# Optimization experiments

Measured on AMD Instinct MI355X. Metric: run time of the kernel, lower is better.

The kernel has to match this reference:

```python
import jax, jax.numpy as jnp
import numpy as np

B = 16384
N_TABLES = 26
N_ROWS = 100000
D = 64


def _mlp(x, params, last_sigmoid=False):
    n = len(params)
    for i, (w, b) in enumerate(params):
        x = x @ w.T + b
        if last_sigmoid and i == n - 1:
            x = jax.nn.sigmoid(x)
        else:
            x = jax.nn.relu(x)
    return x


def setup_inputs() -> dict:
    key = jax.random.key(0)
    ks = jax.random.split(key, 16)

    def glorot(k, m, n):
        return jax.random.normal(k, (m, n), jnp.float32) * np.sqrt(2.0 / (m + n))

    def bias(k, m):
        return jax.random.normal(k, (m,), jnp.float32) * np.sqrt(1.0 / m)

    return {
        "dense_x": jax.random.normal(ks[0], (B, 13), jnp.float32),
        "lS_i": jax.random.randint(ks[1], (N_TABLES, B), 0, N_ROWS, jnp.int64 if jax.config.jax_enable_x64 else jnp.int32),
        "emb_W": jax.random.normal(ks[2], (N_TABLES, N_ROWS, D), jnp.float32) * np.sqrt(1.0 / N_ROWS),
        "bot_w0": glorot(ks[3], 512, 13), "bot_b0": bias(ks[4], 512),
        "bot_w1": glorot(ks[5], 256, 512), "bot_b1": bias(ks[6], 256),
        "bot_w2": glorot(ks[7], 64, 256), "bot_b2": bias(ks[8], 64),
        "top_w0": glorot(ks[9], 512, 415), "top_b0": bias(ks[10], 512),
        "top_w1": glorot(ks[11], 256, 512), "top_b1": bias(ks[12], 256),
        "top_w2": glorot(ks[13], 1, 256), "top_b2": bias(ks[14], 1),
    }


def reference(dense_x, lS_i, emb_W, bot_w0, bot_b0, bot_w1, bot_b1, bot_w2, bot_b2,
              top_w0, top_b0, top_w1, top_b1, top_w2, top_b2):
    # bottom MLP: [B,13] -> [B,64]
    x = _mlp(dense_x, [(bot_w0, bot_b0), (bot_w1, bot_b1), (bot_w2, bot_b2)])

    # embedding lookups: one index per sample per table (EmbeddingBag sum over bag of 1)
    # emb_W: [T, N, D], lS_i: [T, B] -> ly: [T, B, D]
    ly = jnp.take_along_axis(emb_W, lS_i[:, :, None], axis=1)  # [T, B, D]

    # interaction: T = concat(x, ly) -> [B, 27, D]; Z = T T^T; lower-tri (i>j) flatten
    T = jnp.concatenate([x[None], ly], axis=0).transpose(1, 0, 2)  # [B, 27, D]
    Z = jnp.einsum("bnd,bmd->bnm", T, T)  # [B, 27, 27]
    li, lj = jnp.tril_indices(N_TABLES + 1, k=-1)  # same order as torch list comp
    Zflat = Z[:, li, lj]  # [B, 351]
    R = jnp.concatenate([x, Zflat], axis=1)  # [B, 415]

    # top MLP with sigmoid output
    p = _mlp(R, [(top_w0, top_b0), (top_w1, top_b1), (top_w2, top_b2)], last_sigmoid=True)
    return p
```

## Files before the change

kernel.cpp:

```cpp
#include <hip/hip_runtime.h>
#include <hip/hip_bf16.h>
#include <math.h>


#define BATCH 16384
#define NTAB 26
#define NF 27
#define NROWS 100000
#define EDIM 64
#define PAIRS 351
#define RLD 416

template<int BM, int BN, int BK, int TM, int TN, bool VEC, bool RELU>
__global__ __launch_bounds__(256) void gemm_bias_act(
    const float* __restrict__ A, int lda,
    const float* __restrict__ W, int ldw,
    const float* __restrict__ bias,
    float* __restrict__ C, int ldc,
    int M, int N, int K)
{
    __shared__ float As[BK][BM + 4];
    __shared__ float Ws[BK][BN + 4];

    const int tid  = threadIdx.x;
    const int mblk = blockIdx.x * BM;
    const int nblk = blockIdx.y * BN;

    const int tcol = tid % (BN / TN);
    const int trow = tid / (BN / TN);
    const int m0 = trow * TM;
    const int n0 = tcol * TN;

    float acc[TM][TN];
#pragma unroll
    for (int i = 0; i < TM; ++i)
#pragma unroll
        for (int j = 0; j < TN; ++j) acc[i][j] = 0.f;

    const int ktiles = (K + BK - 1) / BK;
    for (int kt = 0; kt < ktiles; ++kt) {
        const int k0 = kt * BK;
        if (VEC) {
#pragma unroll
            for (int i = 0; i < (BM * BK) / (4 * 256); ++i) {
                int idx = tid + i * 256;
                int am = idx / (BK / 4);
                int a4 = idx % (BK / 4);
                float4 v = *(const float4*)&A[(size_t)(mblk + am) * lda + k0 + a4 * 4];
                As[a4 * 4 + 0][am] = v.x;
                As[a4 * 4 + 1][am] = v.y;
                As[a4 * 4 + 2][am] = v.z;
                As[a4 * 4 + 3][am] = v.w;
            }
#pragma unroll
            for (int i = 0; i < (BN * BK) / (4 * 256); ++i) {
                int idx = tid + i * 256;
                int wn = idx / (BK / 4);
                int w4 = idx % (BK / 4);
                float4 v = *(const float4*)&W[(size_t)(nblk + wn) * ldw + k0 + w4 * 4];
                Ws[w4 * 4 + 0][wn] = v.x;
                Ws[w4 * 4 + 1][wn] = v.y;
                Ws[w4 * 4 + 2][wn] = v.z;
                Ws[w4 * 4 + 3][wn] = v.w;
            }
        } else {
#pragma unroll
            for (int i = 0; i < (BM * BK) / 256; ++i) {
                int idx = tid + i * 256;
                int am = idx / BK;
                int ak = idx % BK;
                int gk = k0 + ak;
                float v = 0.f;
                if (gk < K) v = A[(size_t)(mblk + am) * lda + gk];
                As[ak][am] = v;
            }
#pragma unroll
            for (int i = 0; i < (BN * BK) / 256; ++i) {
                int idx = tid + i * 256;
                int wn = idx / BK;
                int wk = idx % BK;
                int gk = k0 + wk;
                float v = 0.f;
                if (gk < K) v = W[(size_t)(nblk + wn) * ldw + gk];
                Ws[wk][wn] = v;
            }
        }
        __syncthreads();

#pragma unroll
        for (int k = 0; k < BK; ++k) {
            float a[TM], b[TN];
            if (VEC) {
#pragma unroll
                for (int i = 0; i < TM; i += 4) {
                    float4 t = *(const float4*)&As[k][m0 + i];
                    a[i] = t.x; a[i + 1] = t.y; a[i + 2] = t.z; a[i + 3] = t.w;
                }
#pragma unroll
                for (int j = 0; j < TN; j += 4) {
                    float4 t = *(const float4*)&Ws[k][n0 + j];
                    b[j] = t.x; b[j + 1] = t.y; b[j + 2] = t.z; b[j + 3] = t.w;
                }
            } else {
#pragma unroll
                for (int i = 0; i < TM; ++i) a[i] = As[k][m0 + i];
#pragma unroll
                for (int j = 0; j < TN; ++j) b[j] = Ws[k][n0 + j];
            }
#pragma unroll
            for (int i = 0; i < TM; ++i)
#pragma unroll
                for (int j = 0; j < TN; ++j)
                    acc[i][j] += a[i] * b[j];
        }
        __syncthreads();
    }

#pragma unroll
    for (int i = 0; i < TM; ++i) {
        int gm = mblk + m0 + i;
        if (VEC) {
#pragma unroll
            for (int j = 0; j < TN; j += 4) {
                int gn = nblk + n0 + j;
                float4 o;
                o.x = acc[i][j + 0] + bias[gn + 0];
                o.y = acc[i][j + 1] + bias[gn + 1];
                o.z = acc[i][j + 2] + bias[gn + 2];
                o.w = acc[i][j + 3] + bias[gn + 3];
                if (RELU) {
                    o.x = o.x > 0.f ? o.x : 0.f;
                    o.y = o.y > 0.f ? o.y : 0.f;
                    o.z = o.z > 0.f ? o.z : 0.f;
                    o.w = o.w > 0.f ? o.w : 0.f;
                }
                *(float4*)&C[(size_t)gm * ldc + gn] = o;
            }
        } else {
#pragma unroll
            for (int j = 0; j < TN; ++j) {
                int gn = nblk + n0 + j;
                float v = acc[i][j] + bias[gn];
                if (RELU) v = v > 0.f ? v : 0.f;
                C[(size_t)gm * ldc + gn] = v;
            }
        }
    }
}

__global__ __launch_bounds__(256) void pad_w0_kernel(
    const float* __restrict__ w, float* __restrict__ wp)
{
    int idx = blockIdx.x * 256 + threadIdx.x;
    if (idx < 512 * 416) {
        int n = idx / 416, k = idx % 416;
        wp[idx] = (k < 415) ? w[n * 415 + k] : 0.f;
    }
}

__global__ __launch_bounds__(256) void interact_kernel(
    const float* __restrict__ emb,
    const int*   __restrict__ lsi,
    float* __restrict__ R)
{
    __shared__ float Tl[4][NF][68];

    const int wave = threadIdx.x >> 6;
    const int lane = threadIdx.x & 63;
    const int b = blockIdx.x * 4 + wave;

    Tl[wave][0][lane] = R[(size_t)b * RLD + lane];
#pragma unroll 2
    for (int t = 0; t < NTAB; ++t) {
        int row = lsi[t * BATCH + b];
        Tl[wave][t + 1][lane] = emb[((size_t)t * NROWS + row) * EDIM + lane];
    }
    __syncthreads();

    for (int p = lane; p < PAIRS; p += 64) {
        int i = (int)((1.0f + sqrtf(1.0f + 8.0f * (float)p)) * 0.5f);
        while (i * (i - 1) / 2 > p) --i;
        while ((i + 1) * i / 2 <= p) ++i;
        int j = p - i * (i - 1) / 2;

        const float4* ri = (const float4*)&Tl[wave][i][0];
        const float4* rj = (const float4*)&Tl[wave][j][0];
        float s = 0.f;
#pragma unroll
        for (int d = 0; d < EDIM / 4; ++d) {
            float4 a = ri[d], c = rj[d];
            s += a.x * c.x + a.y * c.y + a.z * c.z + a.w * c.w;
        }
        R[(size_t)b * RLD + EDIM + p] = s;
    }
    if (lane == 0) R[(size_t)b * RLD + EDIM + PAIRS] = 0.f;
}

__global__ __launch_bounds__(256) void top_final_kernel(
    const float* __restrict__ h,
    const float* __restrict__ w,
    const float* __restrict__ bias,
    float* __restrict__ out)
{
    const int wave = threadIdx.x >> 6;
    const int lane = threadIdx.x & 63;
    const int b = blockIdx.x * 4 + wave;

    const float4* hv = (const float4*)&h[(size_t)b * 256];
    const float4* wv = (const float4*)w;
    float4 a = hv[lane];
    float4 c = wv[lane];
    float s = a.x * c.x + a.y * c.y + a.z * c.z + a.w * c.w;
#pragma unroll
    for (int off = 32; off; off >>= 1) s += __shfl_down(s, off);
    if (lane == 0) {
        float z = s + bias[0];
        out[b] = 1.f / (1.f + expf(-z));
    }
}

extern "C" void kernel_launch(void* const* d_in, const int* in_sizes, int n_in,
                              void* d_out, int out_size, void* d_ws, size_t ws_size,
                              hipStream_t stream)
{
    const float* dense_x = (const float*)d_in[0];
    const int*   lS_i    = (const int*)  d_in[1];
    const float* emb_W   = (const float*)d_in[2];
    const float* bot_w0  = (const float*)d_in[3];
    const float* bot_b0  = (const float*)d_in[4];
    const float* bot_w1  = (const float*)d_in[5];
    const float* bot_b1  = (const float*)d_in[6];
    const float* bot_w2  = (const float*)d_in[7];
    const float* bot_b2  = (const float*)d_in[8];
    const float* top_w0  = (const float*)d_in[9];
    const float* top_b0  = (const float*)d_in[10];
    const float* top_w1  = (const float*)d_in[11];
    const float* top_b1  = (const float*)d_in[12];
    const float* top_w2  = (const float*)d_in[13];
    const float* top_b2  = (const float*)d_in[14];
    float* out = (float*)d_out;

    float* R    = (float*)d_ws;
    float* hA   = R    + (size_t)BATCH * RLD;
    float* hB   = hA   + (size_t)BATCH * 512;
    float* Wpad = hB   + (size_t)BATCH * 256;

    dim3 blk(256);

    pad_w0_kernel<<<dim3((512 * 416 + 255) / 256), blk, 0, stream>>>(top_w0, Wpad);

    gemm_bias_act<128, 64, 16, 8, 4, false, true><<<dim3(BATCH / 128, 512 / 64), blk, 0, stream>>>(
        dense_x, 13, bot_w0, 13, bot_b0, hA, 512, BATCH, 512, 13);
    gemm_bias_act<128, 128, 16, 8, 8, true, true><<<dim3(BATCH / 128, 256 / 128), blk, 0, stream>>>(
        hA, 512, bot_w1, 512, bot_b1, hB, 256, BATCH, 256, 512);
    gemm_bias_act<128, 64, 16, 8, 4, true, true><<<dim3(BATCH / 128, 64 / 64), blk, 0, stream>>>(
        hB, 256, bot_w2, 256, bot_b2, R, RLD, BATCH, 64, 256);

    interact_kernel<<<dim3(BATCH / 4), blk, 0, stream>>>(emb_W, lS_i, R);

    gemm_bias_act<128, 128, 16, 8, 8, true, true><<<dim3(BATCH / 128, 512 / 128), blk, 0, stream>>>(
        R, RLD, Wpad, RLD, top_b0, hA, 512, BATCH, 512, RLD);
    gemm_bias_act<128, 128, 16, 8, 8, true, true><<<dim3(BATCH / 128, 256 / 128), blk, 0, stream>>>(
        hA, 512, top_w1, 512, top_b1, hB, 256, BATCH, 256, 512);
    top_final_kernel<<<dim3(BATCH / 4), blk, 0, stream>>>(hB, top_w2, top_b2, out);
}
```

Measured before the change: 1.055 ms.

## Use split-bf16 MFMA GEMMs for MLP layers with hi/lo activation storage

```diff
diff --git a/kernel.cpp b/kernel.cpp
--- a/kernel.cpp
+++ b/kernel.cpp
@@ -1,5 +1,4 @@
 #include <hip/hip_runtime.h>
-#include <hip/hip_bf16.h>
 #include <math.h>
 
 
@@ -11,165 +10,195 @@
 #define PAIRS 351
 #define RLD 416
 
-template<int BM, int BN, int BK, int TM, int TN, bool VEC, bool RELU>
-__global__ __launch_bounds__(256) void gemm_bias_act(
-    const float* __restrict__ A, int lda,
-    const float* __restrict__ W, int ldw,
+typedef __attribute__((ext_vector_type(4))) float   accfrag_t;
+typedef __attribute__((ext_vector_type(8))) short   bfrag_t;
+typedef __attribute__((ext_vector_type(4))) unsigned short u16x4;
+
+__device__ __forceinline__ unsigned short f32_to_bf16(float f) {
+    unsigned int u = __float_as_uint(f);
+    u += 0x7fffu + ((u >> 16) & 1u);
+    return (unsigned short)(u >> 16);
+}
+__device__ __forceinline__ float bf16_to_f32(unsigned short h) {
+    return __uint_as_float(((unsigned int)h) << 16);
+}
+
+__device__ __forceinline__ void gload16(const void* g, void* l) {
+    __builtin_amdgcn_global_load_lds(
+        (const __attribute__((address_space(1))) unsigned int*)g,
+        (__attribute__((address_space(3))) unsigned int*)l, 16, 0, 0);
+}
+
+template<int BM, int BN, int EPI>
+__global__ __launch_bounds__(256) void gemm_mfma_split(
+    const unsigned short* __restrict__ Ah, const unsigned short* __restrict__ Al, int lda,
+    const unsigned short* __restrict__ Wh, const unsigned short* __restrict__ Wl, int ldw,
     const float* __restrict__ bias,
-    float* __restrict__ C, int ldc,
-    int M, int N, int K)
-{
-    __shared__ float As[BK][BM + 4];
-    __shared__ float Ws[BK][BN + 4];
+    unsigned short* __restrict__ Chi, unsigned short* __restrict__ Clo, int ldc,
+    float* __restrict__ Cf, int ldcf,
+    int K)
+{
+    constexpr int FM = BM / 32;
+    constexpr int FN = BN / 32;
+
+    __shared__ unsigned short sAh[4 * BM * 8];
+    __shared__ unsigned short sAl[4 * BM * 8];
+    __shared__ unsigned short sWh[4 * BN * 8];
+    __shared__ unsigned short sWl[4 * BN * 8];
 
     const int tid  = threadIdx.x;
+    const int lane = tid & 63;
+    const int wid  = tid >> 6;
+    const int wr   = wid >> 1;
+    const int wc   = wid & 1;
+    const int lr   = lane & 15;
+    const int ls   = lane >> 4;
     const int mblk = blockIdx.x * BM;
     const int nblk = blockIdx.y * BN;
 
-    const int tcol = tid % (BN / TN);
-    const int trow = tid / (BN / TN);
-    const int m0 = trow * TM;
-    const int n0 = tcol * TN;
-
-    float acc[TM][TN];
-#pragma unroll
-    for (int i = 0; i < TM; ++i)
-#pragma unroll
-        for (int j = 0; j < TN; ++j) acc[i][j] = 0.f;
-
-    const int ktiles = (K + BK - 1) / BK;
+    accfrag_t acc[FM][FN];
+#pragma unroll
+    for (int mi = 0; mi < FM; ++mi)
+#pragma unroll
+        for (int nj = 0; nj < FN; ++nj) acc[mi][nj] = (accfrag_t)0.f;
+
+    const int ktiles = K >> 5;
     for (int kt = 0; kt < ktiles; ++kt) {
-        const int k0 = kt * BK;
-        if (VEC) {
-#pragma unroll
-            for (int i = 0; i < (BM * BK) / (4 * 256); ++i) {
-                int idx = tid + i * 256;
-                int am = idx / (BK / 4);
-                int a4 = idx % (BK / 4);
-                float4 v = *(const float4*)&A[(size_t)(mblk + am) * lda + k0 + a4 * 4];
-                As[a4 * 4 + 0][am] = v.x;
-                As[a4 * 4 + 1][am] = v.y;
-                As[a4 * 4 + 2][am] = v.z;
-                As[a4 * 4 + 3][am] = v.w;
+        const int k0 = kt * 32;
+#pragma unroll
+        for (int i = 0; i < (4 * BM) / 256; ++i) {
+            int c = tid + i * 256;
+            int slot = c / BM, row = c % BM;
+            size_t go = (size_t)(mblk + row) * lda + k0 + slot * 8;
+            gload16(Ah + go, &sAh[c * 8]);
+            gload16(Al + go, &sAl[c * 8]);
+        }
+#pragma unroll
+        for (int i = 0; i < (4 * BN) / 256; ++i) {
+            int c = tid + i * 256;
+            int slot = c / BN, row = c % BN;
+            size_t go = (size_t)(nblk + row) * ldw + k0 + slot * 8;
+            gload16(Wh + go, &sWh[c * 8]);
+            gload16(Wl + go, &sWl[c * 8]);
+        }
+        __syncthreads();
+
+        bfrag_t ah[FM], al[FM], bh[FN], bl[FN];
+#pragma unroll
+        for (int mi = 0; mi < FM; ++mi) {
+            int r = wr * (BM / 2) + mi * 16 + lr;
+            ah[mi] = *(const bfrag_t*)&sAh[(ls * BM + r) * 8];
+            al[mi] = *(const bfrag_t*)&sAl[(ls * BM + r) * 8];
+        }
+#pragma unroll
+        for (int nj = 0; nj < FN; ++nj) {
+            int cidx = wc * (BN / 2) + nj * 16 + lr;
+            bh[nj] = *(const bfrag_t*)&sWh[(ls * BN + cidx) * 8];
+            bl[nj] = *(const bfrag_t*)&sWl[(ls * BN + cidx) * 8];
+        }
+#pragma unroll
+        for (int mi = 0; mi < FM; ++mi)
+#pragma unroll
+            for (int nj = 0; nj < FN; ++nj) {
+                acc[mi][nj] = __builtin_amdgcn_mfma_f32_16x16x32_bf16(ah[mi], bh[nj], acc[mi][nj], 0, 0, 0);
+                acc[mi][nj] = __builtin_amdgcn_mfma_f32_16x16x32_bf16(ah[mi], bl[nj], acc[mi][nj], 0, 0, 0);
+                acc[mi][nj] = __builtin_amdgcn_mfma_f32_16x16x32_bf16(al[mi], bh[nj], acc[mi][nj], 0, 0, 0);
             }
-#pragma unroll
-            for (int i = 0; i < (BN * BK) / (4 * 256); ++i) {
-                int idx = tid + i * 256;
-                int wn = idx / (BK / 4);
-                int w4 = idx % (BK / 4);
-                float4 v = *(const float4*)&W[(size_t)(nblk + wn) * ldw + k0 + w4 * 4];
-                Ws[w4 * 4 + 0][wn] = v.x;
-                Ws[w4 * 4 + 1][wn] = v.y;
-                Ws[w4 * 4 + 2][wn] = v.z;
-                Ws[w4 * 4 + 3][wn] = v.w;
+        __syncthreads();
+    }
+
+    float bs[FN];
+#pragma unroll
+    for (int nj = 0; nj < FN; ++nj)
+        bs[nj] = bias[nblk + wc * (BN / 2) + nj * 16 + lr];
+
+#pragma unroll
+    for (int mi = 0; mi < FM; ++mi)
+#pragma unroll
+        for (int nj = 0; nj < FN; ++nj) {
+            int col = nblk + wc * (BN / 2) + nj * 16 + lr;
+#pragma unroll
+            for (int j = 0; j < 4; ++j) {
+                int row = mblk + wr * (BM / 2) + mi * 16 + ls * 4 + j;
+                float v = acc[mi][nj][j] + bs[nj];
+                v = v > 0.f ? v : 0.f;
+                if (EPI == 0 || EPI == 1) {
+                    unsigned short h = f32_to_bf16(v);
+                    Chi[(size_t)row * ldc + col] = h;
+                    Clo[(size_t)row * ldc + col] = f32_to_bf16(v - bf16_to_f32(h));
+                }
+                if (EPI == 1 || EPI == 2) {
+                    Cf[(size_t)row * ldcf + col] = v;
+                }
             }
-        } else {
-#pragma unroll
-            for (int i = 0; i < (BM * BK) / 256; ++i) {
-                int idx = tid + i * 256;
-                int am = idx / BK;
-                int ak = idx % BK;
-                int gk = k0 + ak;
-                float v = 0.f;
-                if (gk < K) v = A[(size_t)(mblk + am) * lda + gk];
-                As[ak][am] = v;
-            }
-#pragma unroll
-            for (int i = 0; i < (BN * BK) / 256; ++i) {
-                int idx = tid + i * 256;
-                int wn = idx / BK;
-                int wk = idx % BK;
-                int gk = k0 + wk;
-                float v = 0.f;
-                if (gk < K) v = W[(size_t)(nblk + wn) * ldw + gk];
-                Ws[wk][wn] = v;
-            }
-        }
-        __syncthreads();
-
-#pragma unroll
-        for (int k = 0; k < BK; ++k) {
-            float a[TM], b[TN];
-            if (VEC) {
-#pragma unroll
-                for (int i = 0; i < TM; i += 4) {
-                    float4 t = *(const float4*)&As[k][m0 + i];
-                    a[i] = t.x; a[i + 1] = t.y; a[i + 2] = t.z; a[i + 3] = t.w;
-                }
-#pragma unroll
-                for (int j = 0; j < TN; j += 4) {
-                    float4 t = *(const float4*)&Ws[k][n0 + j];
-                    b[j] = t.x; b[j + 1] = t.y; b[j + 2] = t.z; b[j + 3] = t.w;
-                }
-            } else {
-#pragma unroll
-                for (int i = 0; i < TM; ++i) a[i] = As[k][m0 + i];
-#pragma unroll
-                for (int j = 0; j < TN; ++j) b[j] = Ws[k][n0 + j];
-            }
-#pragma unroll
-            for (int i = 0; i < TM; ++i)
-#pragma unroll
-                for (int j = 0; j < TN; ++j)
-                    acc[i][j] += a[i] * b[j];
-        }
-        __syncthreads();
-    }
-
-#pragma unroll
-    for (int i = 0; i < TM; ++i) {
-        int gm = mblk + m0 + i;
-        if (VEC) {
-#pragma unroll
-            for (int j = 0; j < TN; j += 4) {
-                int gn = nblk + n0 + j;
-                float4 o;
-                o.x = acc[i][j + 0] + bias[gn + 0];
-                o.y = acc[i][j + 1] + bias[gn + 1];
-                o.z = acc[i][j + 2] + bias[gn + 2];
-                o.w = acc[i][j + 3] + bias[gn + 3];
-                if (RELU) {
-                    o.x = o.x > 0.f ? o.x : 0.f;
-                    o.y = o.y > 0.f ? o.y : 0.f;
-                    o.z = o.z > 0.f ? o.z : 0.f;
-                    o.w = o.w > 0.f ? o.w : 0.f;
-                }
-                *(float4*)&C[(size_t)gm * ldc + gn] = o;
-            }
-        } else {
-#pragma unroll
-            for (int j = 0; j < TN; ++j) {
-                int gn = nblk + n0 + j;
-                float v = acc[i][j] + bias[gn];
-                if (RELU) v = v > 0.f ? v : 0.f;
-                C[(size_t)gm * ldc + gn] = v;
-            }
-        }
-    }
-}
-
-__global__ __launch_bounds__(256) void pad_w0_kernel(
-    const float* __restrict__ w, float* __restrict__ wp)
+        }
+}
+
+__global__ __launch_bounds__(256) void decomp_w_kernel(
+    const float* __restrict__ w, unsigned short* __restrict__ hi,
+    unsigned short* __restrict__ lo, int N, int Kin, int Kout)
 {
     int idx = blockIdx.x * 256 + threadIdx.x;
-    if (idx < 512 * 416) {
-        int n = idx / 416, k = idx % 416;
-        wp[idx] = (k < 415) ? w[n * 415 + k] : 0.f;
-    }
+    if (idx >= N * Kout) return;
+    int n = idx / Kout, k = idx - n * Kout;
+    float v = (k < Kin) ? w[(size_t)n * Kin + k] : 0.f;
+    unsigned short h = f32_to_bf16(v);
+    hi[idx] = h;
+    lo[idx] = f32_to_bf16(v - bf16_to_f32(h));
+}
+
+__global__ __launch_bounds__(256) void bot0_kernel(
+    const float* __restrict__ x,
+    const float* __restrict__ w0,
+    const float* __restrict__ b0,
+    unsigned short* __restrict__ oh, unsigned short* __restrict__ ol)
+{
+    __shared__ float Wt[13][512];
+    __shared__ float xs[2][13];
+    __shared__ float bsh[512];
+    const int tid = threadIdx.x;
+    for (int i = tid; i < 13 * 512; i += 256) {
+        int n = i / 13, k = i - n * 13;
+        Wt[k][n] = w0[i];
+    }
+    bsh[tid] = b0[tid];
+    bsh[tid + 256] = b0[tid + 256];
+    const int brow0 = blockIdx.x * 2;
+    if (tid < 26) xs[tid / 13][tid % 13] = x[(size_t)brow0 * 13 + tid];
+    __syncthreads();
+
+    const int bl = tid >> 7;
+    const int n0 = (tid & 127) * 4;
+    const int b  = brow0 + bl;
+    float a0 = bsh[n0], a1 = bsh[n0 + 1], a2 = bsh[n0 + 2], a3 = bsh[n0 + 3];
+#pragma unroll
+    for (int k = 0; k < 13; ++k) {
+        float xv = xs[bl][k];
+        float4 wv = *(const float4*)&Wt[k][n0];
+        a0 += xv * wv.x; a1 += xv * wv.y; a2 += xv * wv.z; a3 += xv * wv.w;
+    }
+    a0 = fmaxf(a0, 0.f); a1 = fmaxf(a1, 0.f); a2 = fmaxf(a2, 0.f); a3 = fmaxf(a3, 0.f);
+    u16x4 h, l;
+    h.x = f32_to_bf16(a0); l.x = f32_to_bf16(a0 - bf16_to_f32(h.x));
+    h.y = f32_to_bf16(a1); l.y = f32_to_bf16(a1 - bf16_to_f32(h.y));
+    h.z = f32_to_bf16(a2); l.z = f32_to_bf16(a2 - bf16_to_f32(h.z));
+    h.w = f32_to_bf16(a3); l.w = f32_to_bf16(a3 - bf16_to_f32(h.w));
+    *(u16x4*)&oh[(size_t)b * 512 + n0] = h;
+    *(u16x4*)&ol[(size_t)b * 512 + n0] = l;
 }
 
 __global__ __launch_bounds__(256) void interact_kernel(
     const float* __restrict__ emb,
     const int*   __restrict__ lsi,
-    float* __restrict__ R)
+    const float* __restrict__ xf,
+    unsigned short* __restrict__ Rhi, unsigned short* __restrict__ Rlo)
 {
     __shared__ float Tl[4][NF][68];
-
     const int wave = threadIdx.x >> 6;
     const int lane = threadIdx.x & 63;
     const int b = blockIdx.x * 4 + wave;
 
-    Tl[wave][0][lane] = R[(size_t)b * RLD + lane];
+    Tl[wave][0][lane] = xf[(size_t)b * EDIM + lane];
 #pragma unroll 2
     for (int t = 0; t < NTAB; ++t) {
         int row = lsi[t * BATCH + b];
@@ -191,9 +220,16 @@
             float4 a = ri[d], c = rj[d];
             s += a.x * c.x + a.y * c.y + a.z * c.z + a.w * c.w;
         }
-        R[(size_t)b * RLD + EDIM + p] = s;
-    }
-    if (lane == 0) R[(size_t)b * RLD + EDIM + PAIRS] = 0.f;
+        size_t o = (size_t)b * RLD + EDIM + p;
+        unsigned short h = f32_to_bf16(s);
+        Rhi[o] = h;
+        Rlo[o] = f32_to_bf16(s - bf16_to_f32(h));
+    }
+    if (lane == 0) {
+        size_t o = (size_t)b * RLD + 415;
+        Rhi[o] = 0;
+        Rlo[o] = 0;
+    }
 }
 
 __global__ __launch_bounds__(256) void top_final_kernel(
@@ -240,27 +276,43 @@
     const float* top_b2  = (const float*)d_in[14];
     float* out = (float*)d_out;
 
-    float* R    = (float*)d_ws;
-    float* hA   = R    + (size_t)BATCH * RLD;
-    float* hB   = hA   + (size_t)BATCH * 512;
-    float* Wpad = hB   + (size_t)BATCH * 256;
+    unsigned short* p = (unsigned short*)d_ws;
+    unsigned short* hAhi = p; p += (size_t)BATCH * 512;
+    unsigned short* hAlo = p; p += (size_t)BATCH * 512;
+    unsigned short* hBhi = p; p += (size_t)BATCH * 256;
+    unsigned short* hBlo = p; p += (size_t)BATCH * 256;
+    unsigned short* Rhi  = p; p += (size_t)BATCH * RLD;
+    unsigned short* Rlo  = p; p += (size_t)BATCH * RLD;
+    float* xf  = (float*)p;
+    float* hBf = xf + (size_t)BATCH * EDIM;
+    unsigned short* q = (unsigned short*)(hBf + (size_t)BATCH * 256);
+    unsigned short* w1h = q; q += 256 * 512;
+    unsigned short* w1l = q; q += 256 * 512;
+    unsigned short* w2h = q; q += 64 * 256;
+    unsigned short* w2l = q; q += 64 * 256;
+    unsigned short* t0h = q; q += 512 * RLD;
+    unsigned short* t0l = q; q += 512 * RLD;
+    unsigned short* t1h = q; q += 256 * 512;
+    unsigned short* t1l = q; q += 256 * 512;
 
     dim3 blk(256);
 
-    pad_w0_kernel<<<dim3((512 * 416 + 255) / 256), blk, 0, stream>>>(top_w0, Wpad);
-
-    gemm_bias_act<128, 64, 16, 8, 4, false, true><<<dim3(BATCH / 128, 512 / 64), blk, 0, stream>>>(
-        dense_x, 13, bot_w0, 13, bot_b0, hA, 512, BATCH, 512, 13);
-    gemm_bias_act<128, 128, 16, 8, 8, true, true><<<dim3(BATCH / 128, 256 / 128), blk, 0, stream>>>(
-        hA, 512, bot_w1, 512, bot_b1, hB, 256, BATCH, 256, 512);
-    gemm_bias_act<128, 64, 16, 8, 4, true, true><<<dim3(BATCH / 128, 64 / 64), blk, 0, stream>>>(
-        hB, 256, bot_w2, 256, bot_b2, R, RLD, BATCH, 64, 256);
-
-    interact_kernel<<<dim3(BATCH / 4), blk, 0, stream>>>(emb_W, lS_i, R);
-
-    gemm_bias_act<128, 128, 16, 8, 8, true, true><<<dim3(BATCH / 128, 512 / 128), blk, 0, stream>>>(
-        R, RLD, Wpad, RLD, top_b0, hA, 512, BATCH, 512, RLD);
-    gemm_bias_act<128, 128, 16, 8, 8, true, true><<<dim3(BATCH / 128, 256 / 128), blk, 0, stream>>>(
-        hA, 512, top_w1, 512, top_b1, hB, 256, BATCH, 256, 512);
-    top_final_kernel<<<dim3(BATCH / 4), blk, 0, stream>>>(hB, top_w2, top_b2, out);
-}
+    decomp_w_kernel<<<dim3((256 * 512 + 255) / 256), blk, 0, stream>>>(bot_w1, w1h, w1l, 256, 512, 512);
+    decomp_w_kernel<<<dim3((64 * 256 + 255) / 256), blk, 0, stream>>>(bot_w2, w2h, w2l, 64, 256, 256);
+    decomp_w_kernel<<<dim3((512 * RLD + 255) / 256), blk, 0, stream>>>(top_w0, t0h, t0l, 512, 415, RLD);
+    decomp_w_kernel<<<dim3((256 * 512 + 255) / 256), blk, 0, stream>>>(top_w1, t1h, t1l, 256, 512, 512);
+
+    bot0_kernel<<<dim3(BATCH / 2), blk, 0, stream>>>(dense_x, bot_w0, bot_b0, hAhi, hAlo);
+    gemm_mfma_split<64, 128, 0><<<dim3(BATCH / 64, 256 / 128), blk, 0, stream>>>(
+        hAhi, hAlo, 512, w1h, w1l, 512, bot_b1, hBhi, hBlo, 256, nullptr, 0, 512);
+    gemm_mfma_split<64, 64, 1><<<dim3(BATCH / 64, 1), blk, 0, stream>>>(
+        hBhi, hBlo, 256, w2h, w2l, 256, bot_b2, Rhi, Rlo, RLD, xf, EDIM, 256);
+
+    interact_kernel<<<dim3(BATCH / 4), blk, 0, stream>>>(emb_W, lS_i, xf, Rhi, Rlo);
+
+    gemm_mfma_split<64, 128, 0><<<dim3(BATCH / 64, 512 / 128), blk, 0, stream>>>(
+        Rhi, Rlo, RLD, t0h, t0l, RLD, top_b0, hAhi, hAlo, 512, nullptr, 0, RLD);
+    gemm_mfma_split<64, 128, 2><<<dim3(BATCH / 64, 256 / 128), blk, 0, stream>>>(
+        hAhi, hAlo, 512, t1h, t1l, 512, top_b1, nullptr, nullptr, 0, hBf, 256, 512);
+    top_final_kernel<<<dim3(BATCH / 4), blk, 0, stream>>>(hBf, top_w2, top_b2, out);
+}
```

New measurement: 967.0 us. 1.09x faster.
